# Kernel tuning notes

Hardware: AMD Instinct MI355X
Metric: run time of the kernel (lower is better)

## Reference

```python
import jax, jax.numpy as jnp
import numpy as np
from jax import lax

B, Z, X, Y = 8, 4, 32, 32
N = Z * X * Y
REAL_SIZE = jnp.array([25.0, 25.0, 4.0], dtype=jnp.float32)
THRESHOLD = 0.5
CUTOFF = 2.0


def setup_inputs() -> dict:
    key = jax.random.key(0)
    k1, k2 = jax.random.split(key)
    pred = jax.random.normal(k1, (B, Z, X, Y, 10), dtype=jnp.float32)
    targ = jax.random.uniform(k2, (B, Z, X, Y, 10), dtype=jnp.float32)
    return {"pred": pred, "targ": targ}


def _grid():
    z, x, y = jnp.meshgrid(jnp.arange(Z), jnp.arange(X), jnp.arange(Y), indexing="ij")
    return jnp.stack([z, x, y], -1).reshape(N, 3).astype(jnp.float32)


def _nms_mask(adj0, a0):
    # Fixed-size masked version of the original iterative suppression:
    # adj0: [N,N] bool, strictly-upper-triangular 'closer than cutoff' graph
    # a0:   [N] bool, currently active (above-threshold) points in conf-desc order
    def step(state):
        a, _ = state
        m = adj0 & a[:, None] & a[None, :]
        mf = m.astype(jnp.float32)
        r = mf.sum(0)                              # restrain_tensor = DIS.sum(0)
        r = r - (r != 0).astype(jnp.float32) @ mf  # subtract suppressed suppressors
        return ((r == 0.0) & a, a.sum())
    def cond(state):
        a, prev = state
        return a.sum() != prev
    a, _ = lax.while_loop(cond, step, (a0, jnp.int32(-1)))
    return a


def _per_batch(pd_conf, pd_pos, pd_R, tg_conf, tg_pos, tg_R):
    # pd_conf/tg_conf: [N]; pd_pos/tg_pos: [N,3] normalized; pd_R/tg_R: [N,3,3]
    pd_active = pd_conf > THRESHOLD
    tg_active = tg_conf > THRESHOLD
    # sort predictions by confidence descending, inactive pushed to the end
    skey = jnp.where(pd_active, pd_conf, -jnp.inf)
    order = jnp.argsort(-skey)
    pd_pos = pd_pos[order]
    pd_R = pd_R[order]
    a0 = pd_active[order]
    # NMS in NORMALIZED coordinates (as in the original module: real_size scaling
    # is applied only AFTER argnms)
    d = jnp.sqrt(jnp.sum((pd_pos[:, None, :] - pd_pos[None, :, :]) ** 2, -1))  # [N,N]
    iu = jnp.arange(N)
    adj0 = (d < CUTOFF) & (iu[:, None] < iu[None, :])
    keep = lax.stop_gradient(_nms_mask(adj0, a0))
    # greedy matching in real coordinates
    pd_r = pd_pos * REAL_SIZE
    tg_r = tg_pos * REAL_SIZE
    dist = jnp.sqrt(jnp.sum((tg_r[:, None, :] - pd_r[None, :, :]) ** 2, -1))  # [N_tg, N_pd]
    within = (dist < CUTOFF) & tg_active[:, None] & keep[None, :]
    has = within.any(0)                 # pred j has at least one target within cutoff
    first_tg = jnp.argmax(within, 0)    # first (lowest-index) matching target per pred
    tp = has.sum().astype(jnp.int32)
    n_pd = keep.sum().astype(jnp.int32)
    n_tg = tg_active.sum().astype(jnp.int32)
    cm = jnp.stack([tp, n_pd - tp, n_tg - tp])  # [matched, unmatched_pred, unmatched_targ]
    # mean rotation-angle error over matched pairs (3 rotation rows each)
    tgRm = tg_R[first_tg]  # [N,3,3]
    cos = jnp.sum(pd_R * tgRm, -1) / (
        jnp.linalg.norm(pd_R, axis=-1) * jnp.linalg.norm(tgRm, axis=-1))
    ang = jnp.arccos(jnp.clip(cos, -1.0, 1.0)) / jnp.pi * 180.0  # [N,3]
    w = has.astype(jnp.float32)[:, None]
    ms = jnp.where(tp > 0,
                   jnp.sum(ang * w) / (3.0 * jnp.maximum(tp, 1).astype(jnp.float32)),
                   0.0)
    return cm, ms


def _forward(pred, targ):
    grid = _grid()
    zxy = jnp.array([Z, X, Y], dtype=jnp.float32)
    def fields(t, is_pred):
        conf = jax.nn.sigmoid(t[..., 0]) if is_pred else t[..., 0]
        conf = conf.reshape(B, N)
        pos = (t[..., 1:4].reshape(B, N, 3) + grid) / zxy  # (off + cell_idx)/ZXY
        rx = t[..., 4:7].reshape(B, N, 3)
        ry = t[..., 7:10].reshape(B, N, 3)
        R = jnp.stack([rx, ry, jnp.cross(rx, ry)], axis=-2)  # [B,N,3,3]
        return conf, pos, R
    pc, pp, pR = fields(pred, True)
    tc, tpos, tR = fields(targ, False)
    cm, ms = jax.vmap(_per_batch)(pc, pp, pR, tc, tpos, tR)
    return cm.reshape(B, 1, 1, 3), ms.reshape(B, 1, 1, 1).astype(jnp.float32)


def reference(pred, targ):
    return _forward(pred, targ)
```

## Files before the change

kernel.cpp:

```cpp
#include <hip/hip_runtime.h>
#include <math.h>

#define NB    8
#define NPTS  4096
#define NTH   1024
#define SPT   4
#define NFILT 16
#define MAXQ  512
#define MAXU  256
#define MAXK  256

__device__ __forceinline__ int blockReduceSumI(int v, int* scr, int tid) {
    #pragma unroll
    for (int o = 32; o > 0; o >>= 1) v += __shfl_down(v, o, 64);
    if ((tid & 63) == 0) scr[tid >> 6] = v;
    __syncthreads();
    if (tid == 0) {
        int s = 0;
        #pragma unroll
        for (int w = 0; w < NTH / 64; ++w) s += scr[w];
        scr[16] = s;
    }
    __syncthreads();
    return scr[16];
}

__device__ __forceinline__ float rowAngleDeg(float a0, float a1, float a2,
                                             float b0, float b1, float b2) {
    float dot = a0 * b0 + a1 * b1 + a2 * b2;
    float na = sqrtf(a0 * a0 + a1 * a1 + a2 * a2);
    float nb = sqrtf(b0 * b0 + b1 * b1 + b2 * b2);
    float c = dot / (na * nb);
    c = fminf(1.0f, fmaxf(-1.0f, c));
    return acosf(c) * 57.29577951308232f;
}

__global__ __launch_bounds__(NTH) void molan_fused(const float* __restrict__ pred,
                                                   const float* __restrict__ targ,
                                                   float* __restrict__ out) {
    __shared__ int   scr_i[32];
    __shared__ float scr_f[16];
    __shared__ int   cnt[4];
    __shared__ unsigned long long f_key[NFILT];
    __shared__ float f_x[NFILT], f_y[NFILT], f_z[NFILT];
    __shared__ unsigned long long q_key[MAXQ];
    __shared__ float q_x[MAXQ], q_y[MAXQ], q_z[MAXQ];
    __shared__ int   q_res[MAXQ];
    __shared__ unsigned long long u_key[MAXU];
    __shared__ float u_x[MAXU], u_y[MAXU], u_z[MAXU];
    __shared__ float k_x[MAXK], k_y[MAXK], k_z[MAXK];
    __shared__ int   k_idx[MAXK];
    __shared__ unsigned int k_match[MAXK];

    const int b = blockIdx.x;
    const int tid = threadIdx.x;
    const float* pb = pred + (size_t)b * NPTS * 10;
    const float* tb = targ + (size_t)b * NPTS * 10;

    unsigned long long key[SPT];
    bool  act[SPT];
    float cx[SPT], cy[SPT], cz[SPT];
    bool  t_act[SPT];
    float t_x[SPT], t_y[SPT], t_z[SPT];
    int loc = 0, loc_t = 0;
    #pragma unroll
    for (int s = 0; s < SPT; ++s) {
        const int n = tid + NTH * s;
        const float2* p2 = (const float2*)(pb + (size_t)n * 10);
        const float2* t2 = (const float2*)(tb + (size_t)n * 10);
        float2 f0 = p2[0];
        float2 f1 = p2[1];
        float2 g0 = t2[0];
        float2 g1 = t2[1];
        const float gz = (float)(n >> 10);
        const float gx = (float)((n >> 5) & 31);
        const float gy = (float)(n & 31);
        float conf = 1.0f / (1.0f + expf(-f0.x));
        bool a = conf > 0.5f;
        act[s] = a;
        loc += a ? 1 : 0;
        unsigned int u = ~(__float_as_uint(conf) | 0x80000000u);
        key[s] = a ? (((unsigned long long)u << 32) | (unsigned int)n)
                   : ~0ull;
        cx[s] = (f0.y + gz) * 0.25f;
        cy[s] = (f1.x + gx) * 0.03125f;
        cz[s] = (f1.y + gy) * 0.03125f;
        bool ta = g0.x > 0.5f;
        t_act[s] = ta;
        loc_t += ta ? 1 : 0;
        t_x[s] = (g0.y + gz) * 6.25f;
        t_y[s] = (g1.x + gx) * 0.78125f;
        t_z[s] = (g1.y + gy) * 0.125f;
    }

    int cur = blockReduceSumI(loc, scr_i, tid);
    int prev = -1;
    bool small_done = false;
    int n_pd = 0;
    while (cur != prev) {
        if (cur <= 64) {
            if (tid == 0) cnt[2] = 0;
            __syncthreads();
            #pragma unroll
            for (int s = 0; s < SPT; ++s) {
                if (act[s]) {
                    int e = atomicAdd(&cnt[2], 1);
                    u_key[e] = key[s]; u_x[e] = cx[s]; u_y[e] = cy[s]; u_z[e] = cz[s];
                }
            }
            __syncthreads();
            if (tid < 64) {
                const int n = cnt[2];
                bool va = tid < n;
                unsigned long long k = va ? u_key[tid] : ~0ull;
                float x = va ? u_x[tid] : 0.f;
                float y = va ? u_y[tid] : 0.f;
                float z = va ? u_z[tid] : 0.f;
                bool a = va;
                int pc = prev, cc = cur;
                while (cc != pc) {
                    unsigned long long am = __ballot(a);
                    bool sfl = false;
                    for (int i = 0; i < n; ++i) {
                        unsigned long long ki = __shfl(k, i, 64);
                        float xi = __shfl(x, i, 64);
                        float yi = __shfl(y, i, 64);
                        float zi = __shfl(z, i, 64);
                        if (((am >> i) & 1ull) && ki < k) {
                            float dx = xi - x, dy = yi - y, dz = zi - z;
                            if (dx * dx + dy * dy + dz * dz < 4.0f) sfl = true;
                        }
                    }
                    unsigned long long rm = __ballot(a && !sfl);
                    bool sp = false;
                    for (int i = 0; i < n; ++i) {
                        if ((rm >> i) & 1ull) {
                            unsigned long long ki = __shfl(k, i, 64);
                            float xi = __shfl(x, i, 64);
                            float yi = __shfl(y, i, 64);
                            float zi = __shfl(z, i, 64);
                            if (ki < k) {
                                float dx = xi - x, dy = yi - y, dz = zi - z;
                                if (dx * dx + dy * dy + dz * dz < 4.0f) sp = true;
                            }
                        }
                    }
                    a = a && !sp;
                    pc = cc;
                    cc = __popcll(__ballot(a));
                }
                unsigned long long fm = __ballot(a);
                int K = __popcll(fm);
                if (tid == 0) { cnt[3] = K; cnt[0] = K; }
                if (a) {
                    int e = __popcll(fm & ((1ull << tid) - 1ull));
                    k_x[e] = x * 25.0f; k_y[e] = y * 25.0f; k_z[e] = z * 4.0f;
                    k_idx[e] = (int)(k & 0xFFFFFFFFull);
                    k_match[e] = 0xFFFFFFFFu;
                }
            }
            __syncthreads();
            n_pd = cnt[0];
            small_done = true;
            break;
        }

        {
            unsigned long long bk = ~0ull;
            float bx = 0.f, by = 0.f, bz = 0.f;
            #pragma unroll
            for (int s = 0; s < SPT; ++s)
                if (act[s] && key[s] < bk) { bk = key[s]; bx = cx[s]; by = cy[s]; bz = cz[s]; }
            #pragma unroll
            for (int o = 32; o > 0; o >>= 1) {
                unsigned long long ok = __shfl_xor(bk, o, 64);
                float ox = __shfl_xor(bx, o, 64);
                float oy = __shfl_xor(by, o, 64);
                float oz = __shfl_xor(bz, o, 64);
                if (ok < bk) { bk = ok; bx = ox; by = oy; bz = oz; }
            }
            if ((tid & 63) == 0) {
                int w = tid >> 6;
                f_key[w] = bk; f_x[w] = bx; f_y[w] = by; f_z[w] = bz;
            }
        }
        __syncthreads();

        bool sflag[SPT], pend[SPT];
        #pragma unroll
        for (int s = 0; s < SPT; ++s) {
            sflag[s] = false; pend[s] = false;
            if (!act[s]) continue;
            bool found = false;
            for (int f = 0; f < NFILT; ++f) {
                if (f_key[f] < key[s]) {
                    float dx = f_x[f] - cx[s], dy = f_y[f] - cy[s], dz = f_z[f] - cz[s];
                    if (dx * dx + dy * dy + dz * dz < 4.0f) { found = true; break; }
                }
            }
            if (found) sflag[s] = true;
            else pend[s] = true;
        }
        do {
            if (tid == 0) cnt[1] = 0;
            __syncthreads();
            int qe[SPT];
            #pragma unroll
            for (int s = 0; s < SPT; ++s) {
                qe[s] = -1;
                if (pend[s]) {
                    int e = atomicAdd(&cnt[1], 1);
                    if (e < MAXQ) {
                        q_key[e] = key[s]; q_x[e] = cx[s]; q_y[e] = cy[s]; q_z[e] = cz[s];
                        q_res[e] = 0;
                        qe[s] = e; pend[s] = false;
                    }
                }
            }
            __syncthreads();
            const int Q = min(cnt[1], MAXQ);
            for (int e = 0; e < Q; ++e) {
                unsigned long long qk = q_key[e];
                float qx = q_x[e], qy = q_y[e], qz = q_z[e];
                bool hit = false;
                #pragma unroll
                for (int s = 0; s < SPT; ++s) {
                    if (act[s] && key[s] < qk) {
                        float dx = cx[s] - qx, dy = cy[s] - qy, dz = cz[s] - qz;
                        if (dx * dx + dy * dy + dz * dz < 4.0f) hit = true;
                    }
                }
                if (hit) q_res[e] = 1;
            }
            __syncthreads();
            #pragma unroll
            for (int s = 0; s < SPT; ++s)
                if (qe[s] >= 0) sflag[s] = (q_res[qe[s]] != 0);
        } while (cnt[1] > MAXQ);

        bool upend[SPT], supp[SPT];
        #pragma unroll
        for (int s = 0; s < SPT; ++s) {
            upend[s] = act[s] && !sflag[s];
            supp[s] = false;
        }
        do {
            if (tid == 0) cnt[2] = 0;
            __syncthreads();
            #pragma unroll
            for (int s = 0; s < SPT; ++s) {
                if (upend[s]) {
                    int e = atomicAdd(&cnt[2], 1);
                    if (e < MAXU) {
                        u_key[e] = key[s]; u_x[e] = cx[s]; u_y[e] = cy[s]; u_z[e] = cz[s];
                        upend[s] = false;
                    }
                }
            }
            __syncthreads();
            const int Ku = min(cnt[2], MAXU);
            #pragma unroll
            for (int s = 0; s < SPT; ++s) {
                if (!act[s] || supp[s]) continue;
                for (int e = 0; e < Ku; ++e) {
                    if (u_key[e] < key[s]) {
                        float dx = u_x[e] - cx[s], dy = u_y[e] - cy[s], dz = u_z[e] - cz[s];
                        if (dx * dx + dy * dy + dz * dz < 4.0f) { supp[s] = true; break; }
                    }
                }
            }
        } while (cnt[2] > MAXU);
        loc = 0;
        #pragma unroll
        for (int s = 0; s < SPT; ++s) {
            if (act[s] && supp[s]) act[s] = false;
            loc += act[s] ? 1 : 0;
        }
        prev = cur;
        cur = blockReduceSumI(loc, scr_i, tid);
    }
    if (!small_done) n_pd = cur;

    bool kpend[SPT];
    #pragma unroll
    for (int s = 0; s < SPT; ++s) kpend[s] = small_done ? false : act[s];
    int loc_tp = 0;
    float loc_ang = 0.0f;
    do {
        if (tid == 0 && !small_done) cnt[3] = 0;
        __syncthreads();
        #pragma unroll
        for (int s = 0; s < SPT; ++s) {
            if (kpend[s]) {
                int e = atomicAdd(&cnt[3], 1);
                if (e < MAXK) {
                    k_x[e] = cx[s] * 25.0f; k_y[e] = cy[s] * 25.0f; k_z[e] = cz[s] * 4.0f;
                    k_idx[e] = tid + NTH * s;
                    k_match[e] = 0xFFFFFFFFu;
                    kpend[s] = false;
                }
            }
        }
        __syncthreads();
        const int K = min(cnt[3], MAXK);
        #pragma unroll
        for (int s = 0; s < SPT; ++s) {
            if (!t_act[s]) continue;
            float tx = t_x[s], ty = t_y[s], tz = t_z[s];
            for (int e = 0; e < K; ++e) {
                float dx = tx - k_x[e], dy = ty - k_y[e], dz = tz - k_z[e];
                if (dx * dx + dy * dy + dz * dz < 4.0f)
                    atomicMin(&k_match[e], (unsigned int)(tid + NTH * s));
            }
        }
        __syncthreads();
        if (tid < K) {
            unsigned int m = k_match[tid];
            if (m != 0xFFFFFFFFu) {
                ++loc_tp;
                const float2* pr = (const float2*)(pb + (size_t)k_idx[tid] * 10 + 4);
                float2 p0 = pr[0], p1 = pr[1], p2v = pr[2];
                float ax0 = p0.x, ax1 = p0.y, ax2 = p1.x;
                float ay0 = p1.y, ay1 = p2v.x, ay2 = p2v.y;
                float az0 = ax1 * ay2 - ax2 * ay1;
                float az1 = ax2 * ay0 - ax0 * ay2;
                float az2 = ax0 * ay1 - ax1 * ay0;
                const float2* tr = (const float2*)(tb + (size_t)m * 10 + 4);
                float2 t0 = tr[0], t1 = tr[1], t2v = tr[2];
                float bx0 = t0.x, bx1 = t0.y, bx2 = t1.x;
                float by0 = t1.y, by1 = t2v.x, by2 = t2v.y;
                float bz0 = bx1 * by2 - bx2 * by1;
                float bz1 = bx2 * by0 - bx0 * by2;
                float bz2 = bx0 * by1 - bx1 * by0;
                loc_ang += rowAngleDeg(ax0, ax1, ax2, bx0, bx1, bx2);
                loc_ang += rowAngleDeg(ay0, ay1, ay2, by0, by1, by2);
                loc_ang += rowAngleDeg(az0, az1, az2, bz0, bz1, bz2);
            }
        }
    } while (cnt[3] > MAXK);

    {
        int v0 = loc_tp, v1 = loc_t;
        float vf = loc_ang;
        #pragma unroll
        for (int o = 32; o > 0; o >>= 1) {
            v0 += __shfl_down(v0, o, 64);
            v1 += __shfl_down(v1, o, 64);
            vf += __shfl_down(vf, o, 64);
        }
        if ((tid & 63) == 0) {
            int w = tid >> 6;
            scr_i[w] = v0; scr_i[16 + w] = v1; scr_f[w] = vf;
        }
        __syncthreads();
        if (tid == 0) {
            int tp = 0, nt = 0;
            float angsum = 0.0f;
            #pragma unroll
            for (int w = 0; w < NTH / 64; ++w) {
                tp += scr_i[w]; nt += scr_i[16 + w]; angsum += scr_f[w];
            }
            out[b * 3 + 0] = (float)tp;
            out[b * 3 + 1] = (float)(n_pd - tp);
            out[b * 3 + 2] = (float)(nt - tp);
            out[NB * 3 + b] = (tp > 0) ? (angsum / (3.0f * (float)tp)) : 0.0f;
        }
    }
}

extern "C" void kernel_launch(void* const* d_in, const int* in_sizes, int n_in,
                              void* d_out, int out_size, void* d_ws, size_t ws_size,
                              hipStream_t stream) {
    const float* pred = (const float*)d_in[0];
    const float* targ = (const float*)d_in[1];
    float* out = (float*)d_out;
    (void)d_ws; (void)ws_size;
    molan_fused<<<dim3(NB), dim3(NTH), 0, stream>>>(pred, targ, out);
}
```

Measured before the change: 70.06 us.

## Spread input decode across 64 cooperative blocks and compact active points before NMS

The kernel becomes a cooperative launch of 64 blocks. All blocks decode the pred and targ points in parallel, stream-compact the active ones per 256-point chunk into workspace, and then a grid sync lets only the 8 per-batch blocks run NMS and matching on the compacted records. This is meant to remove the serial load and decode done by just 8 blocks and to pack active points densely. In exchange it adds a grid-wide barrier, workspace round-trips and the overhead of a cooperative launch, and it now relies on a workspace being provided.

```diff
diff --git a/kernel.cpp b/kernel.cpp
--- a/kernel.cpp
+++ b/kernel.cpp
@@ -1,14 +1,24 @@
 #include <hip/hip_runtime.h>
+#include <hip/hip_cooperative_groups.h>
 #include <math.h>
+
+namespace cg = cooperative_groups;
 
 #define NB    8
 #define NPTS  4096
 #define NTH   1024
+#define NBLK  64
 #define SPT   4
 #define NFILT 16
 #define MAXQ  512
 #define MAXU  256
 #define MAXK  256
+
+#define WS_PCC  0
+#define WS_TCC  512
+#define WS_PKEY 1024
+#define WS_PPOS 263168
+#define WS_TPOS 787456
 
 __device__ __forceinline__ int blockReduceSumI(int v, int* scr, int tid) {
     #pragma unroll
@@ -35,12 +45,15 @@
     return acosf(c) * 57.29577951308232f;
 }
 
-__global__ __launch_bounds__(NTH) void molan_fused(const float* __restrict__ pred,
-                                                   const float* __restrict__ targ,
-                                                   float* __restrict__ out) {
+__global__ __launch_bounds__(NTH) void molan_coop(const float* __restrict__ pred,
+                                                  const float* __restrict__ targ,
+                                                  unsigned char* __restrict__ ws,
+                                                  float* __restrict__ out) {
+    __shared__ int   wcnt[16];
     __shared__ int   scr_i[32];
     __shared__ float scr_f[16];
     __shared__ int   cnt[4];
+    __shared__ int   ccP[16], ccT[16];
     __shared__ unsigned long long f_key[NFILT];
     __shared__ float f_x[NFILT], f_y[NFILT], f_z[NFILT];
     __shared__ unsigned long long q_key[MAXQ];
@@ -52,48 +65,115 @@
     __shared__ int   k_idx[MAXK];
     __shared__ unsigned int k_match[MAXK];
 
-    const int b = blockIdx.x;
+    unsigned int* pcc = (unsigned int*)(ws + WS_PCC);
+    unsigned int* tcc = (unsigned int*)(ws + WS_TCC);
+    unsigned long long* pkeyw = (unsigned long long*)(ws + WS_PKEY);
+    float4* pposw = (float4*)(ws + WS_PPOS);
+    float4* tposw = (float4*)(ws + WS_TPOS);
+
     const int tid = threadIdx.x;
-    const float* pb = pred + (size_t)b * NPTS * 10;
-    const float* tb = targ + (size_t)b * NPTS * 10;
-
-    unsigned long long key[SPT];
-    bool  act[SPT];
-    float cx[SPT], cy[SPT], cz[SPT];
-    bool  t_act[SPT];
-    float t_x[SPT], t_y[SPT], t_z[SPT];
-    int loc = 0, loc_t = 0;
-    #pragma unroll
-    for (int s = 0; s < SPT; ++s) {
-        const int n = tid + NTH * s;
-        const float2* p2 = (const float2*)(pb + (size_t)n * 10);
-        const float2* t2 = (const float2*)(tb + (size_t)n * 10);
-        float2 f0 = p2[0];
-        float2 f1 = p2[1];
-        float2 g0 = t2[0];
-        float2 g1 = t2[1];
+
+    {
+        const int gid = blockIdx.x * NTH + tid;
+        const int tensor = gid >> 15;
+        const int batch = (gid >> 12) & 7;
+        const int n = gid & 4095;
+        const float* base = (tensor ? targ : pred)
+                            + (size_t)batch * NPTS * 10 + (size_t)n * 10;
+        float2 f0 = *(const float2*)base;
+        float2 f1 = *(const float2*)(base + 2);
         const float gz = (float)(n >> 10);
         const float gx = (float)((n >> 5) & 31);
         const float gy = (float)(n & 31);
-        float conf = 1.0f / (1.0f + expf(-f0.x));
-        bool a = conf > 0.5f;
+
+        bool active;
+        unsigned long long key = 0;
+        float4 rec;
+        if (tensor == 0) {
+            float conf = 1.0f / (1.0f + expf(-f0.x));
+            active = conf > 0.5f;
+            unsigned int u = ~(__float_as_uint(conf) | 0x80000000u);
+            key = ((unsigned long long)u << 32) | (unsigned int)n;
+            rec = make_float4((f0.y + gz) * 0.25f,
+                              (f1.x + gx) * 0.03125f,
+                              (f1.y + gy) * 0.03125f,
+                              (float)n);
+        } else {
+            active = f0.x > 0.5f;
+            rec = make_float4((f0.y + gz) * 6.25f,
+                              (f1.x + gx) * 0.78125f,
+                              (f1.y + gy) * 0.125f,
+                              (float)n);
+        }
+
+        const int lane = tid & 63, wid = tid >> 6;
+        unsigned long long ball = __ballot(active);
+        int lofs = __popcll(ball & ((1ull << lane) - 1ull));
+        if (lane == 0) wcnt[wid] = __popcll(ball);
+        __syncthreads();
+        int wb = 0;
+        for (int w = wid & ~3; w < wid; ++w) wb += wcnt[w];
+        const int chunk = n >> 8;
+        if ((tid & 255) == 0) {
+            int c = wcnt[wid] + wcnt[wid + 1] + wcnt[wid + 2] + wcnt[wid + 3];
+            (tensor ? tcc : pcc)[batch * 16 + chunk] = (unsigned int)c;
+        }
+        if (active) {
+            int e = batch * NPTS + chunk * 256 + wb + lofs;
+            if (tensor == 0) { pkeyw[e] = key; pposw[e] = rec; }
+            else tposw[e] = rec;
+        }
+    }
+    __threadfence();
+    cg::this_grid().sync();
+    if (blockIdx.x >= NB) return;
+
+    const int b = blockIdx.x;
+    const float* pb = pred + (size_t)b * NPTS * 10;
+    const float* tb = targ + (size_t)b * NPTS * 10;
+    const unsigned long long* pkey_r = pkeyw + b * NPTS;
+    const float4* ppos_r = pposw + b * NPTS;
+    const float4* tpos_r = tposw + b * NPTS;
+
+    if (tid < 16) ccP[tid] = (int)pcc[b * 16 + tid];
+    else if (tid < 32) ccT[tid - 16] = (int)tcc[b * 16 + tid - 16];
+    __syncthreads();
+
+    unsigned long long key[SPT];
+    bool  act[SPT];
+    int   pidx[SPT];
+    float cx[SPT], cy[SPT], cz[SPT];
+    #pragma unroll
+    for (int s = 0; s < SPT; ++s) {
+        int slot = tid + NTH * s;
+        bool a = (slot & 255) < ccP[slot >> 8];
         act[s] = a;
-        loc += a ? 1 : 0;
-        unsigned int u = ~(__float_as_uint(conf) | 0x80000000u);
-        key[s] = a ? (((unsigned long long)u << 32) | (unsigned int)n)
-                   : ~0ull;
-        cx[s] = (f0.y + gz) * 0.25f;
-        cy[s] = (f1.x + gx) * 0.03125f;
-        cz[s] = (f1.y + gy) * 0.03125f;
-        bool ta = g0.x > 0.5f;
-        t_act[s] = ta;
-        loc_t += ta ? 1 : 0;
-        t_x[s] = (g0.y + gz) * 6.25f;
-        t_y[s] = (g1.x + gx) * 0.78125f;
-        t_z[s] = (g1.y + gy) * 0.125f;
-    }
-
-    int cur = blockReduceSumI(loc, scr_i, tid);
+        key[s] = ~0ull;
+        cx[s] = cy[s] = cz[s] = 0.f; pidx[s] = 0;
+        if (a) {
+            key[s] = pkey_r[slot];
+            float4 p = ppos_r[slot];
+            cx[s] = p.x; cy[s] = p.y; cz[s] = p.z; pidx[s] = (int)p.w;
+        }
+    }
+    bool  t_act[SPT];
+    int   t_n[SPT];
+    float t_x[SPT], t_y[SPT], t_z[SPT];
+    #pragma unroll
+    for (int s = 0; s < SPT; ++s) {
+        int slot = tid + NTH * s;
+        bool a = (slot & 255) < ccT[slot >> 8];
+        t_act[s] = a;
+        t_x[s] = t_y[s] = t_z[s] = 0.f; t_n[s] = 0;
+        if (a) {
+            float4 p = tpos_r[slot];
+            t_x[s] = p.x; t_y[s] = p.y; t_z[s] = p.z; t_n[s] = (int)p.w;
+        }
+    }
+
+    int cur = 0;
+    #pragma unroll
+    for (int c = 0; c < 16; ++c) cur += ccP[c];
     int prev = -1;
     bool small_done = false;
     int n_pd = 0;
@@ -270,7 +350,7 @@
                 }
             }
         } while (cnt[2] > MAXU);
-        loc = 0;
+        int loc = 0;
         #pragma unroll
         for (int s = 0; s < SPT; ++s) {
             if (act[s] && supp[s]) act[s] = false;
@@ -295,7 +375,7 @@
                 int e = atomicAdd(&cnt[3], 1);
                 if (e < MAXK) {
                     k_x[e] = cx[s] * 25.0f; k_y[e] = cy[s] * 25.0f; k_z[e] = cz[s] * 4.0f;
-                    k_idx[e] = tid + NTH * s;
+                    k_idx[e] = pidx[s];
                     k_match[e] = 0xFFFFFFFFu;
                     kpend[s] = false;
                 }
@@ -310,7 +390,7 @@
             for (int e = 0; e < K; ++e) {
                 float dx = tx - k_x[e], dy = ty - k_y[e], dz = tz - k_z[e];
                 if (dx * dx + dy * dy + dz * dz < 4.0f)
-                    atomicMin(&k_match[e], (unsigned int)(tid + NTH * s));
+                    atomicMin(&k_match[e], (unsigned int)t_n[s]);
             }
         }
         __syncthreads();
@@ -340,26 +420,25 @@
     } while (cnt[3] > MAXK);
 
     {
-        int v0 = loc_tp, v1 = loc_t;
+        int v0 = loc_tp;
         float vf = loc_ang;
         #pragma unroll
         for (int o = 32; o > 0; o >>= 1) {
             v0 += __shfl_down(v0, o, 64);
-            v1 += __shfl_down(v1, o, 64);
             vf += __shfl_down(vf, o, 64);
         }
         if ((tid & 63) == 0) {
             int w = tid >> 6;
-            scr_i[w] = v0; scr_i[16 + w] = v1; scr_f[w] = vf;
+            scr_i[w] = v0; scr_f[w] = vf;
         }
         __syncthreads();
         if (tid == 0) {
             int tp = 0, nt = 0;
             float angsum = 0.0f;
             #pragma unroll
-            for (int w = 0; w < NTH / 64; ++w) {
-                tp += scr_i[w]; nt += scr_i[16 + w]; angsum += scr_f[w];
-            }
+            for (int w = 0; w < NTH / 64; ++w) { tp += scr_i[w]; angsum += scr_f[w]; }
+            #pragma unroll
+            for (int c = 0; c < 16; ++c) nt += ccT[c];
             out[b * 3 + 0] = (float)tp;
             out[b * 3 + 1] = (float)(n_pd - tp);
             out[b * 3 + 2] = (float)(nt - tp);
@@ -374,6 +453,7 @@
     const float* pred = (const float*)d_in[0];
     const float* targ = (const float*)d_in[1];
     float* out = (float*)d_out;
-    (void)d_ws; (void)ws_size;
-    molan_fused<<<dim3(NB), dim3(NTH), 0, stream>>>(pred, targ, out);
+    unsigned char* ws = (unsigned char*)d_ws;
+    void* args[] = {(void*)&pred, (void*)&targ, (void*)&ws, (void*)&out};
+    hipLaunchCooperativeKernel((void*)molan_coop, dim3(NBLK), dim3(NTH), args, 0, stream);
 }
```

New measurement: 111.6 us. 1.59x slower.
